# Kernel tuning notes

Measured on AMD Instinct MI355X. Metric: run time of the kernel, lower is better.

The kernel has to match this reference:

```python
import jax, jax.numpy as jnp
import numpy as np

B, LQ, LKV = 4, 512, 8192
Q_DIM, KV_DIM = 1024, 512
QK_CH, V_CH, N_HEADS = 256, 256, 8
EPS = 1e-5


def _layernorm(x, g, b):
    m = jnp.mean(x, axis=-1, keepdims=True)
    v = jnp.mean(jnp.square(x - m), axis=-1, keepdims=True)
    return (x - m) * jax.lax.rsqrt(v + EPS) * g + b


def setup_inputs() -> dict:
    key = jax.random.key(0)
    ks = jax.random.split(key, 8)
    hidden_states = jax.random.normal(ks[0], (B, LQ, Q_DIM), dtype=jnp.float32)
    inputs = jax.random.normal(ks[1], (B, LKV, KV_DIM), dtype=jnp.float32)
    # Linear weights stored as [in, out] for x @ W
    Wq = jax.random.normal(ks[2], (Q_DIM, QK_CH), dtype=jnp.float32) * (1.0 / np.sqrt(Q_DIM))
    Wk = jax.random.normal(ks[3], (KV_DIM, QK_CH), dtype=jnp.float32) * (1.0 / np.sqrt(KV_DIM))
    Wv = jax.random.normal(ks[4], (KV_DIM, V_CH), dtype=jnp.float32) * (1.0 / np.sqrt(KV_DIM))
    bq = jnp.zeros((QK_CH,), jnp.float32)
    bk = jax.random.normal(ks[5], (QK_CH,), dtype=jnp.float32) * 0.02
    bv = jax.random.normal(ks[6], (V_CH,), dtype=jnp.float32) * 0.02
    ln1_g = jnp.ones((Q_DIM,), jnp.float32)
    ln1_b = jnp.zeros((Q_DIM,), jnp.float32)
    ln2_g = jnp.ones((KV_DIM,), jnp.float32)
    ln2_b = jnp.zeros((KV_DIM,), jnp.float32)
    return dict(hidden_states=hidden_states, inputs=inputs,
                ln1_g=ln1_g, ln1_b=ln1_b, ln2_g=ln2_g, ln2_b=ln2_b,
                Wq=Wq, bq=bq, Wk=Wk, bk=bk, Wv=Wv, bv=bv)


def reference(hidden_states, inputs, ln1_g, ln1_b, ln2_g, ln2_b,
              Wq, bq, Wk, bk, Wv, bv):
    H = N_HEADS
    dqk = QK_CH // H
    dv = V_CH // H
    hs = _layernorm(hidden_states, ln1_g, ln1_b)          # [B,LQ,Q_DIM]
    inp = _layernorm(inputs, ln2_g, ln2_b)                # [B,LKV,KV_DIM]
    q = (hs @ Wq + bq).reshape(B, LQ, H, dqk)             # [B,LQ,H,dqk]
    k = (inp @ Wk + bk).reshape(B, LKV, H, dqk)           # [B,LKV,H,dqk]
    v = (inp @ Wv + bv).reshape(B, LKV, H, dv)            # [B,LKV,H,dv]
    scores = jnp.einsum('bqhd,bkhd->bhqk', q, k) / np.sqrt(dqk).astype(np.float32)
    probs = jax.nn.softmax(scores, axis=-1)               # [B,H,LQ,LKV] (materialized, as in torch)
    ctx = jnp.einsum('bhqk,bkhd->bqhd', probs, v)         # [B,LQ,H,dv]
    return ctx.reshape(B, LQ, H * dv)
```

## Files before the change

### kernel.cpp

```cpp
#include <hip/hip_runtime.h>
#include <hip/hip_bf16.h>
#include <math.h>

#define NB    4
#define LQ    512
#define LKV   8192
#define QDIM  1024
#define KVDIM 512
#define NH    8
#define EPS_LN 1e-5f
#define SMAX  12.0f

typedef __attribute__((ext_vector_type(8))) short bf16x8;
typedef __attribute__((ext_vector_type(4))) float f32x4;

static __device__ __forceinline__ ushort f2bf(float x) {
    unsigned int u = __builtin_bit_cast(unsigned int, x);
    u += 0x7FFFu + ((u >> 16) & 1u);
    return (ushort)(u >> 16);
}

#if __has_builtin(__builtin_amdgcn_cvt_pk_bf16_f32)
static __device__ __forceinline__ unsigned int pk_bf16(float a, float b) {
    auto r = __builtin_amdgcn_cvt_pk_bf16_f32(a, b);
    return __builtin_bit_cast(unsigned int, r);
}
#else
static __device__ __forceinline__ unsigned int pk_bf16(float a, float b) {
    return (unsigned int)f2bf(a) | ((unsigned int)f2bf(b) << 16);
}
#endif

#if __has_builtin(__builtin_amdgcn_exp2f)
#define EXP2F(x) __builtin_amdgcn_exp2f(x)
#else
#define EXP2F(x) exp2f(x)
#endif

static __device__ __forceinline__ void interleave_swap(unsigned int &x, unsigned int &y, int lane) {
#if __has_builtin(__builtin_amdgcn_permlane32_swap) && __has_builtin(__builtin_amdgcn_permlane16_swap)
    {
        auto r1 = __builtin_amdgcn_permlane32_swap(x, y, false, false);
        auto r2 = __builtin_amdgcn_permlane16_swap(r1[0], r1[1], false, false);
        x = (unsigned int)r2[0];
        y = (unsigned int)r2[1];
    }
#else
    {
        unsigned int xs = (unsigned int)__shfl_xor((int)x, 32, 64);
        unsigned int ys = (unsigned int)__shfl_xor((int)y, 32, 64);
        unsigned int A2 = (lane & 32) ? ys : x;
        unsigned int C2 = (lane & 32) ? y  : xs;
        unsigned int A2x = (unsigned int)__shfl_xor((int)A2, 16, 64);
        unsigned int C2x = (unsigned int)__shfl_xor((int)C2, 16, 64);
        x = (lane & 16) ? C2x : A2;
        y = (lane & 16) ? C2  : A2x;
    }
#endif
}

static __device__ __forceinline__ void gld_lds16(const ushort* g, ushort* l) {
    __builtin_amdgcn_global_load_lds(
        (const __attribute__((address_space(1))) unsigned int*)g,
        (__attribute__((address_space(3))) unsigned int*)l, 16, 0, 0);
}

template<int K>
static __device__ __forceinline__ void ln_norm_row(
    const float* __restrict__ x, const float* __restrict__ g,
    const float* __restrict__ bta, ushort* __restrict__ y, int row, int lane)
{
    const float* xp = x + (size_t)row * K;
    constexpr int NV = K / 256;
    float4 v[NV];
    float s = 0.f;
#pragma unroll
    for (int i = 0; i < NV; ++i) {
        v[i] = *(const float4*)(xp + lane * 4 + i * 256);
        s += v[i].x + v[i].y + v[i].z + v[i].w;
    }
#pragma unroll
    for (int o = 1; o < 64; o <<= 1) s += __shfl_xor(s, o, 64);
    const float mu = s * (1.0f / K);
    float vs = 0.f;
#pragma unroll
    for (int i = 0; i < NV; ++i) {
        float dx = v[i].x - mu, dy = v[i].y - mu, dz = v[i].z - mu, dw = v[i].w - mu;
        vs += dx * dx + dy * dy + dz * dz + dw * dw;
    }
#pragma unroll
    for (int o = 1; o < 64; o <<= 1) vs += __shfl_xor(vs, o, 64);
    const float rs = rsqrtf(vs * (1.0f / K) + EPS_LN);
#pragma unroll
    for (int i = 0; i < NV; ++i) {
        const float4 gv = *(const float4*)(g   + lane * 4 + i * 256);
        const float4 bv = *(const float4*)(bta + lane * 4 + i * 256);
        uint2 o;
        o.x = pk_bf16((v[i].x - mu) * rs * gv.x + bv.x, (v[i].y - mu) * rs * gv.y + bv.y);
        o.y = pk_bf16((v[i].z - mu) * rs * gv.z + bv.z, (v[i].w - mu) * rs * gv.w + bv.w);
        *(uint2*)(y + (size_t)row * K + lane * 4 + i * 256) = o;
    }
}

static __device__ __forceinline__ void ln_stats_row(
    const float* __restrict__ x, float* __restrict__ mean, float* __restrict__ rstd,
    int row, int lane)
{
    const float* xp = x + (size_t)row * QDIM;
    float4 v[4];
    float s = 0.f;
#pragma unroll
    for (int i = 0; i < 4; ++i) {
        v[i] = *(const float4*)(xp + lane * 4 + i * 256);
        s += v[i].x + v[i].y + v[i].z + v[i].w;
    }
#pragma unroll
    for (int o = 1; o < 64; o <<= 1) s += __shfl_xor(s, o, 64);
    const float mu = s * (1.0f / QDIM);
    float vs = 0.f;
#pragma unroll
    for (int i = 0; i < 4; ++i) {
        float dx = v[i].x - mu, dy = v[i].y - mu, dz = v[i].z - mu, dw = v[i].w - mu;
        vs += dx * dx + dy * dy + dz * dz + dw * dw;
    }
#pragma unroll
    for (int o = 1; o < 64; o <<= 1) vs += __shfl_xor(vs, o, 64);
    if (lane == 0) {
        mean[row] = mu;
        rstd[row] = rsqrtf(vs * (1.0f / QDIM) + EPS_LN);
    }
}

static __device__ __forceinline__ void wt_transpose_body(
    const float* __restrict__ src, ushort* __restrict__ dst, int K,
    int kx, int ny, int t, ushort (*Ts)[72])
{
    const int k0 = kx * 64, n0 = ny * 64;
    const int nl = t & 63;
#pragma unroll
    for (int p = 0; p < 16; ++p) {
        const int kl = p * 4 + (t >> 6);
        Ts[nl][kl] = f2bf(src[(size_t)(k0 + kl) * 256 + n0 + nl]);
    }
    __syncthreads();
    const int ck = (t & 7) * 8;
#pragma unroll
    for (int p = 0; p < 2; ++p) {
        const int rn = p * 32 + (t >> 3);
        *(bf16x8*)(dst + (size_t)(n0 + rn) * K + k0 + ck) = *(const bf16x8*)&Ts[rn][ck];
    }
}

__global__ __launch_bounds__(256) void phaseA_kernel(
    const float* __restrict__ inputs, const float* __restrict__ ln2g,
    const float* __restrict__ ln2b,   ushort* __restrict__ Abf,
    const float* __restrict__ hidden, float* __restrict__ mean_h, float* __restrict__ rstd_h,
    const float* __restrict__ Wq, const float* __restrict__ Wk, const float* __restrict__ Wv,
    ushort* __restrict__ WtQ, ushort* __restrict__ WtKV)
{
    __shared__ ushort Ts[64][72];
    const int bid = blockIdx.x;
    const int t = threadIdx.x;
    const int lane = t & 63;
    if (bid < 8192) {
        ln_norm_row<KVDIM>(inputs, ln2g, ln2b, Abf, bid * 4 + (t >> 6), lane);
    } else if (bid < 8704) {
        ln_stats_row(hidden, mean_h, rstd_h, (bid - 8192) * 4 + (t >> 6), lane);
    } else if (bid < 8768) {
        const int p = bid - 8704;
        wt_transpose_body(Wq, WtQ, QDIM, p & 15, p >> 4, t, Ts);
    } else if (bid < 8800) {
        const int p = bid - 8768;
        wt_transpose_body(Wk, WtKV, KVDIM, p & 7, p >> 3, t, Ts);
    } else {
        const int p = bid - 8800;
        wt_transpose_body(Wv, WtKV + (size_t)256 * KVDIM, KVDIM, p & 7, p >> 3, t, Ts);
    }
}

__global__ __launch_bounds__(256, 3) void phaseB_kernel(
    const ushort* __restrict__ Abf, const ushort* __restrict__ WtKV,
    const float* __restrict__ bk, const float* __restrict__ bv,
    ushort* __restrict__ kb, ushort* __restrict__ vt,
    const float* __restrict__ hidden, const float* __restrict__ mean_h,
    const float* __restrict__ rstd_h,
    const float* __restrict__ ln1g, const float* __restrict__ ln1b,
    const ushort* __restrict__ WtQ, const float* __restrict__ bq,
    ushort* __restrict__ qb, float oscale)
{
    __shared__ __align__(16) ushort SMEM[24576];
    const int bid  = blockIdx.x;
    const int t    = threadIdx.x;
    const int lane = t & 63;
    const int w    = t >> 6;
    const int lq   = lane & 15;
    const int lg   = lane >> 4;
    const int wm   = w >> 1;
    const int wn   = w & 1;

    if (bid < 2048) {
        const int work = ((bid & 7) << 8) | (bid >> 3);
        const int bm = (work >> 2) * 64;
        const int bn = (work & 3) * 128;

        const int srow = t >> 3;
        const int scol = ((t & 7) ^ (srow & 7)) * 8;
        const ushort* gA = Abf  + (size_t)(bm + srow) * KVDIM + scol;
        const ushort* gB = WtKV + (size_t)(bn + srow) * KVDIM + scol;

#define STAGE_KV(buf, k0) do {                                              \
        ushort* a_ = SMEM + (buf) * 4096;                                   \
        ushort* b_ = SMEM + 8192 + (buf) * 8192;                            \
        gld_lds16(gA + (k0),                          a_ + t * 8);          \
        gld_lds16(gA + (size_t)32 * KVDIM + (k0),     a_ + 2048 + t * 8);   \
        gld_lds16(gB + (k0),                          b_ + t * 8);          \
        gld_lds16(gB + (size_t)32 * KVDIM + (k0),     b_ + 2048 + t * 8);   \
        gld_lds16(gB + (size_t)64 * KVDIM + (k0),     b_ + 4096 + t * 8);   \
        gld_lds16(gB + (size_t)96 * KVDIM + (k0),     b_ + 6144 + t * 8);   \
    } while (0)

        f32x4 acc[4][2] = {};
        STAGE_KV(0, 0);
        __syncthreads();
        for (int i = 0; i < 8; ++i) {
            const int cur = i & 1;
            if (i < 7) STAGE_KV(cur ^ 1, (i + 1) * 64);
            const ushort* a_ = SMEM + cur * 4096;
            const ushort* b_ = SMEM + 8192 + cur * 8192;
#pragma unroll
            for (int kh = 0; kh < 2; ++kh) {
                bf16x8 af[4], bf[2];
#pragma unroll
                for (int mt = 0; mt < 4; ++mt) {
                    const int m = mt * 16 + lq;
                    af[mt] = *(const bf16x8*)(a_ + m * 64 + (((lg + 4 * kh) ^ (m & 7)) << 3));
                }
#pragma unroll
                for (int nt = 0; nt < 2; ++nt) {
                    const int n = w * 32 + nt * 16 + lq;
                    bf[nt] = *(const bf16x8*)(b_ + n * 64 + (((lg + 4 * kh) ^ (n & 7)) << 3));
                }
#pragma unroll
                for (int mt = 0; mt < 4; ++mt)
#pragma unroll
                    for (int nt = 0; nt < 2; ++nt)
                        acc[mt][nt] = __builtin_amdgcn_mfma_f32_16x16x32_bf16(af[mt], bf[nt], acc[mt][nt], 0, 0, 0);
            }
            __syncthreads();
        }
#undef STAGE_KV
        const int bidx = bm >> 13;
        const int tokb = bm & 8191;
        const int nc0  = bn + w * 32;

        if (bn < 256) {
            ushort* Cs = SMEM + w * 2560;
#pragma unroll
            for (int nt = 0; nt < 2; ++nt) {
                const int n_l = nt * 16 + lq;
                const float bias = bk[nc0 + n_l];
#pragma unroll
                for (int mt = 0; mt < 4; ++mt)
#pragma unroll
                    for (int r = 0; r < 4; ++r)
                        Cs[(mt * 16 + lg * 4 + r) * 40 + n_l] = f2bf(acc[mt][nt][r] + bias);
            }
            const int r0 = lane >> 2;
            const int ck = (lane & 3) * 8;
            const int h  = nc0 >> 5;
            const size_t obase = (((size_t)(bidx * NH + h) << 13) + tokb) * 32 + ck;
#pragma unroll
            for (int p = 0; p < 4; ++p) {
                const int row = p * 16 + r0;
                *(bf16x8*)(kb + obase + (size_t)row * 32) = *(const bf16x8*)&Cs[row * 40 + ck];
            }
        } else {
            ushort* Cs = SMEM + w * 2560;
#pragma unroll
            for (int nt = 0; nt < 2; ++nt) {
                const int n_l = nt * 16 + lq;
                const float bias = bv[(nc0 - 256) + n_l];
#pragma unroll
                for (int mt = 0; mt < 4; ++mt) {
                    uint2 o;
                    o.x = pk_bf16(acc[mt][nt][0] + bias, acc[mt][nt][1] + bias);
                    o.y = pk_bf16(acc[mt][nt][2] + bias, acc[mt][nt][3] + bias);
                    *(uint2*)&Cs[n_l * 72 + mt * 16 + lg * 4] = o;
                }
            }
            const int r0 = lane >> 3;
            const int cm = (lane & 7) * 8;
            const int nv0 = nc0 - 256;
            const int h  = nv0 >> 5;
            const int tokc = tokb + cm;
#pragma unroll
            for (int p = 0; p < 4; ++p) {
                const int row = p * 8 + r0;
                *(bf16x8*)(vt + ((size_t)(bidx * NH + h) * 32 + row) * LKV + tokc) =
                    *(const bf16x8*)&Cs[row * 72 + cm];
            }
        }
    } else {
        const int p  = bid - 2048;
        const int bm = (p >> 2) * 64;
        const int bn = (p & 3) * 64;
        ushort* As = SMEM;
        ushort* Bs = SMEM + 4096;

        const int srow = t >> 3;
        const int scol = ((t & 7) ^ (srow & 7)) * 8;
        const ushort* gB = WtQ + (size_t)(bn + srow) * QDIM + scol;
        ushort* lB  = Bs + t * 8;
        ushort* lA0 = As + t * 8;
        ushort* lA1 = As + 2048 + t * 8;

        const int r0 = bm + srow;
        const float mu0 = mean_h[r0],      rs0 = rstd_h[r0];
        const float mu1 = mean_h[r0 + 32], rs1 = rstd_h[r0 + 32];
        const float* xA0 = hidden + (size_t)r0 * QDIM + scol;
        const float* xA1 = xA0 + (size_t)32 * QDIM;

        f32x4 acc[2][2] = {};
        for (int k0 = 0; k0 < QDIM; k0 += 64) {
            gld_lds16(gB + k0,                      lB);
            gld_lds16(gB + (size_t)32 * QDIM + k0,  lB + 2048);
            const float4 a0 = *(const float4*)(xA0 + k0);
            const float4 a1 = *(const float4*)(xA0 + k0 + 4);
            const float4 c0 = *(const float4*)(xA1 + k0);
            const float4 c1 = *(const float4*)(xA1 + k0 + 4);
            const float4 g0 = *(const float4*)(ln1g + k0 + scol);
            const float4 g1 = *(const float4*)(ln1g + k0 + scol + 4);
            const float4 d0 = *(const float4*)(ln1b + k0 + scol);
            const float4 d1 = *(const float4*)(ln1b + k0 + scol + 4);
            uint4 w0, w1;
            w0.x = pk_bf16((a0.x - mu0) * rs0 * g0.x + d0.x, (a0.y - mu0) * rs0 * g0.y + d0.y);
            w0.y = pk_bf16((a0.z - mu0) * rs0 * g0.z + d0.z, (a0.w - mu0) * rs0 * g0.w + d0.w);
            w0.z = pk_bf16((a1.x - mu0) * rs0 * g1.x + d1.x, (a1.y - mu0) * rs0 * g1.y + d1.y);
            w0.w = pk_bf16((a1.z - mu0) * rs0 * g1.z + d1.z, (a1.w - mu0) * rs0 * g1.w + d1.w);
            w1.x = pk_bf16((c0.x - mu1) * rs1 * g0.x + d0.x, (c0.y - mu1) * rs1 * g0.y + d0.y);
            w1.y = pk_bf16((c0.z - mu1) * rs1 * g0.z + d0.z, (c0.w - mu1) * rs1 * g0.w + d0.w);
            w1.z = pk_bf16((c1.x - mu1) * rs1 * g1.x + d1.x, (c1.y - mu1) * rs1 * g1.y + d1.y);
            w1.w = pk_bf16((c1.z - mu1) * rs1 * g1.z + d1.z, (c1.w - mu1) * rs1 * g1.w + d1.w);
            *(uint4*)lA0 = w0;
            *(uint4*)lA1 = w1;
            __syncthreads();
#pragma unroll
            for (int kh = 0; kh < 2; ++kh) {
                bf16x8 af[2], bf[2];
#pragma unroll
                for (int mt = 0; mt < 2; ++mt) {
                    const int m = wm * 32 + mt * 16 + lq;
                    af[mt] = *(const bf16x8*)(As + m * 64 + (((lg + 4 * kh) ^ (m & 7)) << 3));
                }
#pragma unroll
                for (int nt = 0; nt < 2; ++nt) {
                    const int n = wn * 32 + nt * 16 + lq;
                    bf[nt] = *(const bf16x8*)(Bs + n * 64 + (((lg + 4 * kh) ^ (n & 7)) << 3));
                }
#pragma unroll
                for (int mt = 0; mt < 2; ++mt)
#pragma unroll
                    for (int nt = 0; nt < 2; ++nt)
                        acc[mt][nt] = __builtin_amdgcn_mfma_f32_16x16x32_bf16(af[mt], bf[nt], acc[mt][nt], 0, 0, 0);
            }
            __syncthreads();
        }

#pragma unroll
        for (int nt = 0; nt < 2; ++nt) {
            const int n = bn + wn * 32 + nt * 16 + lq;
            const int h = n >> 5, d = n & 31;
            const float bias = bq[n];
#pragma unroll
            for (int mt = 0; mt < 2; ++mt) {
                const int m0   = bm + wm * 32 + mt * 16 + lg * 4;
                const int bidx = m0 >> 9;
                const int tok  = m0 & 511;
                const size_t base = (((size_t)(bidx * NH + h) << 9) + tok) * 32 + d;
#pragma unroll
                for (int r = 0; r < 4; ++r)
                    qb[base + (size_t)r * 32] = f2bf((acc[mt][nt][r] + bias) * oscale);
            }
        }
    }
}

#define NQ 8
__global__ __launch_bounds__(256, 2) void attn_mfma_kernel(
    const ushort* __restrict__ Qb,
    const ushort* __restrict__ Kb,
    const ushort* __restrict__ Vt,
    float* __restrict__ Opart,
    float* __restrict__ lpart)
{
    const int bid = blockIdx.x;
    const int xcd = bid & 7;
    const int u   = bid >> 3;
    const int bhw = u >> 4;
    const int r2  = u & 15;
    const int qt  = r2 >> 2;
    const int quarter = r2 & 3;
    const int bh  = (bhw << 3) | xcd;
    const int t = threadIdx.x, w = t >> 6, lane = t & 63;
    const int lq = lane & 15, lg = lane >> 4;

    __shared__ __align__(16) float Ob[2 * 128 * 36];
    __shared__ float lbuf[4][128];

    bf16x8 qfrag[NQ];
    const size_t qbase = ((size_t)bh * LQ + qt * 128) * 32;
#pragma unroll
    for (int n = 0; n < NQ; ++n)
        qfrag[n] = *(const bf16x8*)(Qb + qbase + (size_t)(n * 16 + lq) * 32 + lg * 8);

    const int kv0 = quarter * 2048 + w * 512;
    const ushort* KpA = Kb + ((size_t)bh * LKV + kv0 + lq) * 32 + lg * 8;
    const ushort* VpA = Vt + ((size_t)bh * 32 + lq) * LKV + kv0 + lg * 8;

    f32x4 oacc[2][NQ] = {};
    float l_part[NQ] = {};
    const f32x4 cM = {-SMAX, -SMAX, -SMAX, -SMAX};

    for (int kt = 0; kt < 512; kt += 64) {
        bf16x8 kc[4];
#pragma unroll
        for (int m = 0; m < 4; ++m)
            kc[m] = *(const bf16x8*)(KpA + (size_t)(kt + m * 16) * 32);
        bf16x8 vc[2][2];
#pragma unroll
        for (int dt = 0; dt < 2; ++dt)
#pragma unroll
            for (int z = 0; z < 2; ++z)
                vc[dt][z] = *(const bf16x8*)(VpA + (size_t)(dt * 16) * LKV + kt + z * 32);

#pragma unroll
        for (int z = 0; z < 2; ++z) {
#pragma unroll
            for (int n = 0; n < NQ; ++n) {
                f32x4 s0 = __builtin_amdgcn_mfma_f32_16x16x32_bf16(kc[2 * z],     qfrag[n], cM, 0, 0, 0);
                f32x4 s1 = __builtin_amdgcn_mfma_f32_16x16x32_bf16(kc[2 * z + 1], qfrag[n], cM, 0, 0, 0);
                const float e0 = EXP2F(s0[0]);
                const float e1 = EXP2F(s0[1]);
                const float e2 = EXP2F(s0[2]);
                const float e3 = EXP2F(s0[3]);
                const float f0 = EXP2F(s1[0]);
                const float f1 = EXP2F(s1[1]);
                const float f2 = EXP2F(s1[2]);
                const float f3 = EXP2F(s1[3]);
                l_part[n] += ((e0 + e1) + (e2 + e3)) + ((f0 + f1) + (f2 + f3));
                unsigned int wa = pk_bf16(e0, e1);
                unsigned int wb = pk_bf16(e2, e3);
                unsigned int wc = pk_bf16(f0, f1);
                unsigned int wd = pk_bf16(f2, f3);
                interleave_swap(wa, wc, lane);
                interleave_swap(wb, wd, lane);
                uint4 wv;
                wv.x = wa; wv.y = wb; wv.z = wc; wv.w = wd;
                const bf16x8 pfz = __builtin_bit_cast(bf16x8, wv);
                oacc[0][n] = __builtin_amdgcn_mfma_f32_16x16x32_bf16(vc[0][z], pfz, oacc[0][n], 0, 0, 0);
                oacc[1][n] = __builtin_amdgcn_mfma_f32_16x16x32_bf16(vc[1][z], pfz, oacc[1][n], 0, 0, 0);
            }
        }
    }

#pragma unroll
    for (int n = 0; n < NQ; ++n) {
        l_part[n] += __shfl_xor(l_part[n], 16);
        l_part[n] += __shfl_xor(l_part[n], 32);
    }
    if (lg == 0) {
#pragma unroll
        for (int n = 0; n < NQ; ++n)
            lbuf[w][n * 16 + lq] = l_part[n];
    }
    if (w >= 2) {
#pragma unroll
        for (int n = 0; n < NQ; ++n)
#pragma unroll
            for (int dt = 0; dt < 2; ++dt)
                *(f32x4*)&Ob[((size_t)(w - 2) * 128 + n * 16 + lq) * 36 + dt * 16 + lg * 4] = oacc[dt][n];
    }
    __syncthreads();
    if (w < 2) {
#pragma unroll
        for (int n = 0; n < NQ; ++n)
#pragma unroll
            for (int dt = 0; dt < 2; ++dt) {
                float* p = &Ob[((size_t)w * 128 + n * 16 + lq) * 36 + dt * 16 + lg * 4];
                f32x4 v = *(f32x4*)p;
                v += oacc[dt][n];
                *(f32x4*)p = v;
            }
    }
    __syncthreads();
    {
        const int pidx = (quarter * 32 + bh) * 4 + qt;
        const int q  = t >> 3;
        const int d0 = (t & 7) * 4;
#pragma unroll
        for (int rh = 0; rh < 4; ++rh) {
            const int row = q + rh * 32;
            f32x4 s0 = *(const f32x4*)&Ob[((size_t)row) * 36 + d0];
            f32x4 s1 = *(const f32x4*)&Ob[((size_t)(128 + row)) * 36 + d0];
            s0 += s1;
            *(f32x4*)(Opart + (size_t)pidx * 4096 + row * 32 + d0) = s0;
            if ((t & 7) == 0) {
                float gl = lbuf[0][row] + lbuf[1][row] + lbuf[2][row] + lbuf[3][row];
                lpart[(size_t)pidx * 128 + row] = gl;
            }
        }
    }
}

__global__ __launch_bounds__(256) void attn_combine_kernel(
    const float* __restrict__ Opart, const float* __restrict__ lpart,
    float* __restrict__ Out)
{
    const int cb = blockIdx.x;
    const int bh = cb >> 2, qt = cb & 3;
    const int b = bh >> 3, h = bh & 7;
    const int t = threadIdx.x;
    const int q = t >> 3;
    const int dq = (t & 7) * 4;
#pragma unroll
    for (int rh = 0; rh < 4; ++rh) {
        const int row = q + rh * 32;
        float4 o = {0.f, 0.f, 0.f, 0.f};
        float l = 0.f;
#pragma unroll
        for (int j = 0; j < 4; ++j) {
            const size_t pidx = (size_t)((j * 32 + bh) * 4 + qt);
            const float4 a = *(const float4*)(Opart + pidx * 4096 + row * 32 + dq);
            o.x += a.x; o.y += a.y; o.z += a.z; o.w += a.w;
            l += lpart[pidx * 128 + row];
        }
        const float inv = 1.0f / l;
        o.x *= inv; o.y *= inv; o.z *= inv; o.w *= inv;
        *(float4*)(Out + ((size_t)b * LQ + qt * 128 + row) * 256 + h * 32 + dq) = o;
    }
}

extern "C" void kernel_launch(void* const* d_in, const int* in_sizes, int n_in,
                              void* d_out, int out_size, void* d_ws, size_t ws_size,
                              hipStream_t stream)
{
    const float* hidden = (const float*)d_in[0];
    const float* inputs = (const float*)d_in[1];
    const float* ln1g   = (const float*)d_in[2];
    const float* ln1b   = (const float*)d_in[3];
    const float* ln2g   = (const float*)d_in[4];
    const float* ln2b   = (const float*)d_in[5];
    const float* Wq     = (const float*)d_in[6];
    const float* bq     = (const float*)d_in[7];
    const float* Wk     = (const float*)d_in[8];
    const float* bk     = (const float*)d_in[9];
    const float* Wv     = (const float*)d_in[10];
    const float* bv     = (const float*)d_in[11];
    float* out = (float*)d_out;

    char* wsb = (char*)d_ws;
    ushort* qb     = (ushort*)(wsb);
    ushort* WtKV   = (ushort*)(wsb + (1u << 20));
    ushort* WtQ    = (ushort*)(wsb + (1u << 20) + (512u << 10));
    float*  mean_h = (float*)(wsb + (2u << 20));
    float*  rstd_h = (float*)(wsb + (2u << 20) + 8192);
    ushort* kb     = (ushort*)(wsb + (2u << 20) + 16384);
    ushort* vt     = (ushort*)(wsb + (18u << 20) + 16384);
    ushort* Abf    = (ushort*)(wsb + (34u << 20) + 16384);

    float* Opart = (float*)Abf;
    float* lpart = Opart + (size_t)4 * 32 * 4 * 4096;

    const float oscale = 0.2550540226496112f;

    phaseA_kernel<<<8832, 256, 0, stream>>>(inputs, ln2g, ln2b, Abf,
                                            hidden, mean_h, rstd_h,
                                            Wq, Wk, Wv, WtQ, WtKV);
    phaseB_kernel<<<2176, 256, 0, stream>>>(Abf, WtKV, bk, bv, kb, vt,
                                            hidden, mean_h, rstd_h, ln1g, ln1b,
                                            WtQ, bq, qb, oscale);
    attn_mfma_kernel<<<512, 256, 0, stream>>>(qb, kb, vt, Opart, lpart);
    attn_combine_kernel<<<128, 256, 0, stream>>>(Opart, lpart, out);
}
```

Baseline: 199.2 us.

## Enlarge KV projection tiles to 128x256 with 512-thread blocks

After: 202.9 us. Within noise of the previous version (+1.8%).

```diff
diff --git a/kernel.cpp b/kernel.cpp
--- a/kernel.cpp
+++ b/kernel.cpp
@@ -178,7 +178,7 @@
     }
 }
 
-__global__ __launch_bounds__(256, 3) void phaseB_kernel(
+__global__ __launch_bounds__(512, 2) void phaseB_kernel(
     const ushort* __restrict__ Abf, const ushort* __restrict__ WtKV,
     const float* __restrict__ bk, const float* __restrict__ bv,
     ushort* __restrict__ kb, ushort* __restrict__ vt,
@@ -195,113 +195,111 @@
     const int w    = t >> 6;
     const int lq   = lane & 15;
     const int lg   = lane >> 4;
-    const int wm   = w >> 1;
-    const int wn   = w & 1;
-
-    if (bid < 2048) {
-        const int work = ((bid & 7) << 8) | (bid >> 3);
-        const int bm = (work >> 2) * 64;
-        const int bn = (work & 3) * 128;
-
-        const int srow = t >> 3;
-        const int scol = ((t & 7) ^ (srow & 7)) * 8;
+    const int wm   = w >> 2;
+    const int wn   = w & 3;
+
+    if (bid < 512) {
+        const int work = ((bid & 7) << 6) | (bid >> 3);
+        const int bm = (work >> 1) * 128;
+        const int bn = (work & 1) * 256;
+
+        const int srow = t >> 2;
+        const int scol = ((t & 3) ^ ((t >> 3) & 3)) * 8;
         const ushort* gA = Abf  + (size_t)(bm + srow) * KVDIM + scol;
         const ushort* gB = WtKV + (size_t)(bn + srow) * KVDIM + scol;
 
-#define STAGE_KV(buf, k0) do {                                              \
-        ushort* a_ = SMEM + (buf) * 4096;                                   \
-        ushort* b_ = SMEM + 8192 + (buf) * 8192;                            \
-        gld_lds16(gA + (k0),                          a_ + t * 8);          \
-        gld_lds16(gA + (size_t)32 * KVDIM + (k0),     a_ + 2048 + t * 8);   \
-        gld_lds16(gB + (k0),                          b_ + t * 8);          \
-        gld_lds16(gB + (size_t)32 * KVDIM + (k0),     b_ + 2048 + t * 8);   \
-        gld_lds16(gB + (size_t)64 * KVDIM + (k0),     b_ + 4096 + t * 8);   \
-        gld_lds16(gB + (size_t)96 * KVDIM + (k0),     b_ + 6144 + t * 8);   \
+#define STAGE_KV(buf, k0) do {                                            \
+        ushort* a_ = SMEM + (buf) * 4096;                                 \
+        ushort* b_ = SMEM + 8192 + (buf) * 8192;                          \
+        gld_lds16(gA + (k0),                       a_ + t * 8);           \
+        gld_lds16(gB + (k0),                       b_ + t * 8);           \
+        gld_lds16(gB + (size_t)128 * KVDIM + (k0), b_ + 4096 + t * 8);    \
     } while (0)
 
-        f32x4 acc[4][2] = {};
+        f32x4 acc[4][4] = {};
         STAGE_KV(0, 0);
         __syncthreads();
-        for (int i = 0; i < 8; ++i) {
+        for (int i = 0; i < 16; ++i) {
             const int cur = i & 1;
-            if (i < 7) STAGE_KV(cur ^ 1, (i + 1) * 64);
+            if (i < 15) STAGE_KV(cur ^ 1, (i + 1) * 32);
             const ushort* a_ = SMEM + cur * 4096;
             const ushort* b_ = SMEM + 8192 + cur * 8192;
-#pragma unroll
-            for (int kh = 0; kh < 2; ++kh) {
-                bf16x8 af[4], bf[2];
-#pragma unroll
-                for (int mt = 0; mt < 4; ++mt) {
-                    const int m = mt * 16 + lq;
-                    af[mt] = *(const bf16x8*)(a_ + m * 64 + (((lg + 4 * kh) ^ (m & 7)) << 3));
-                }
-#pragma unroll
-                for (int nt = 0; nt < 2; ++nt) {
-                    const int n = w * 32 + nt * 16 + lq;
-                    bf[nt] = *(const bf16x8*)(b_ + n * 64 + (((lg + 4 * kh) ^ (n & 7)) << 3));
-                }
-#pragma unroll
-                for (int mt = 0; mt < 4; ++mt)
-#pragma unroll
-                    for (int nt = 0; nt < 2; ++nt)
-                        acc[mt][nt] = __builtin_amdgcn_mfma_f32_16x16x32_bf16(af[mt], bf[nt], acc[mt][nt], 0, 0, 0);
-            }
+            bf16x8 af[4], bf[4];
+#pragma unroll
+            for (int mt = 0; mt < 4; ++mt) {
+                const int m = wm * 64 + mt * 16 + lq;
+                af[mt] = *(const bf16x8*)(a_ + m * 32 + ((lg ^ ((m >> 1) & 3)) << 3));
+            }
+#pragma unroll
+            for (int nt = 0; nt < 4; ++nt) {
+                const int n = wn * 64 + nt * 16 + lq;
+                bf[nt] = *(const bf16x8*)(b_ + n * 32 + ((lg ^ ((n >> 1) & 3)) << 3));
+            }
+#pragma unroll
+            for (int mt = 0; mt < 4; ++mt)
+#pragma unroll
+                for (int nt = 0; nt < 4; ++nt)
+                    acc[mt][nt] = __builtin_amdgcn_mfma_f32_16x16x32_bf16(af[mt], bf[nt], acc[mt][nt], 0, 0, 0);
             __syncthreads();
         }
 #undef STAGE_KV
         const int bidx = bm >> 13;
-        const int tokb = bm & 8191;
-        const int nc0  = bn + w * 32;
-
-        if (bn < 256) {
-            ushort* Cs = SMEM + w * 2560;
-#pragma unroll
-            for (int nt = 0; nt < 2; ++nt) {
-                const int n_l = nt * 16 + lq;
-                const float bias = bk[nc0 + n_l];
-#pragma unroll
-                for (int mt = 0; mt < 4; ++mt)
-#pragma unroll
-                    for (int r = 0; r < 4; ++r)
-                        Cs[(mt * 16 + lg * 4 + r) * 40 + n_l] = f2bf(acc[mt][nt][r] + bias);
-            }
-            const int r0 = lane >> 2;
-            const int ck = (lane & 3) * 8;
-            const int h  = nc0 >> 5;
-            const size_t obase = (((size_t)(bidx * NH + h) << 13) + tokb) * 32 + ck;
-#pragma unroll
-            for (int p = 0; p < 4; ++p) {
-                const int row = p * 16 + r0;
-                *(bf16x8*)(kb + obase + (size_t)row * 32) = *(const bf16x8*)&Cs[row * 40 + ck];
+        const int tokb = (bm & 8191) + wm * 64;
+        ushort* Cs = SMEM + w * 2560;
+
+        if (bn == 0) {
+#pragma unroll
+            for (int ch = 0; ch < 2; ++ch) {
+                const int c0 = wn * 64 + ch * 32;
+                const int h  = c0 >> 5;
+#pragma unroll
+                for (int ntr = 0; ntr < 2; ++ntr) {
+                    const int n_l = ntr * 16 + lq;
+                    const float bias = bk[c0 + n_l];
+#pragma unroll
+                    for (int mt = 0; mt < 4; ++mt)
+#pragma unroll
+                        for (int r = 0; r < 4; ++r)
+                            Cs[(mt * 16 + lg * 4 + r) * 40 + n_l] = f2bf(acc[mt][ch * 2 + ntr][r] + bias);
+                }
+                const int r0s = lane >> 2;
+                const int ck  = (lane & 3) * 8;
+                const size_t obase = (((size_t)(bidx * NH + h) << 13) + tokb) * 32 + ck;
+#pragma unroll
+                for (int p = 0; p < 4; ++p) {
+                    const int row = p * 16 + r0s;
+                    *(bf16x8*)(kb + obase + (size_t)row * 32) = *(const bf16x8*)&Cs[row * 40 + ck];
+                }
             }
         } else {
-            ushort* Cs = SMEM + w * 2560;
-#pragma unroll
-            for (int nt = 0; nt < 2; ++nt) {
-                const int n_l = nt * 16 + lq;
-                const float bias = bv[(nc0 - 256) + n_l];
-#pragma unroll
-                for (int mt = 0; mt < 4; ++mt) {
-                    uint2 o;
-                    o.x = pk_bf16(acc[mt][nt][0] + bias, acc[mt][nt][1] + bias);
-                    o.y = pk_bf16(acc[mt][nt][2] + bias, acc[mt][nt][3] + bias);
-                    *(uint2*)&Cs[n_l * 72 + mt * 16 + lg * 4] = o;
+#pragma unroll
+            for (int ch = 0; ch < 2; ++ch) {
+                const int c0 = wn * 64 + ch * 32;
+                const int h  = c0 >> 5;
+#pragma unroll
+                for (int ntr = 0; ntr < 2; ++ntr) {
+                    const int n_l = ntr * 16 + lq;
+                    const float bias = bv[c0 + n_l];
+#pragma unroll
+                    for (int mt = 0; mt < 4; ++mt) {
+                        uint2 o;
+                        o.x = pk_bf16(acc[mt][ch * 2 + ntr][0] + bias, acc[mt][ch * 2 + ntr][1] + bias);
+                        o.y = pk_bf16(acc[mt][ch * 2 + ntr][2] + bias, acc[mt][ch * 2 + ntr][3] + bias);
+                        *(uint2*)&Cs[n_l * 72 + mt * 16 + lg * 4] = o;
+                    }
                 }
-            }
-            const int r0 = lane >> 3;
-            const int cm = (lane & 7) * 8;
-            const int nv0 = nc0 - 256;
-            const int h  = nv0 >> 5;
-            const int tokc = tokb + cm;
-#pragma unroll
-            for (int p = 0; p < 4; ++p) {
-                const int row = p * 8 + r0;
-                *(bf16x8*)(vt + ((size_t)(bidx * NH + h) * 32 + row) * LKV + tokc) =
-                    *(const bf16x8*)&Cs[row * 72 + cm];
+                const int r0s = lane >> 3;
+                const int cm  = (lane & 7) * 8;
+#pragma unroll
+                for (int p = 0; p < 4; ++p) {
+                    const int row = p * 8 + r0s;
+                    *(bf16x8*)(vt + ((size_t)(bidx * NH + h) * 32 + row) * LKV + tokb + cm) =
+                        *(const bf16x8*)&Cs[row * 72 + cm];
+                }
             }
         }
     } else {
-        const int p  = bid - 2048;
+        const int p  = bid - 512;
         const int bm = (p >> 2) * 64;
         const int bn = (p & 3) * 64;
         ushort* As = SMEM;
@@ -310,65 +308,50 @@
         const int srow = t >> 3;
         const int scol = ((t & 7) ^ (srow & 7)) * 8;
         const ushort* gB = WtQ + (size_t)(bn + srow) * QDIM + scol;
-        ushort* lB  = Bs + t * 8;
-        ushort* lA0 = As + t * 8;
-        ushort* lA1 = As + 2048 + t * 8;
+        ushort* lB = Bs + t * 8;
+        ushort* lA = As + t * 8;
 
         const int r0 = bm + srow;
-        const float mu0 = mean_h[r0],      rs0 = rstd_h[r0];
-        const float mu1 = mean_h[r0 + 32], rs1 = rstd_h[r0 + 32];
-        const float* xA0 = hidden + (size_t)r0 * QDIM + scol;
-        const float* xA1 = xA0 + (size_t)32 * QDIM;
-
-        f32x4 acc[2][2] = {};
+        const float mu = mean_h[r0], rs = rstd_h[r0];
+        const float* xA = hidden + (size_t)r0 * QDIM + scol;
+
+        f32x4 acc[2] = {};
         for (int k0 = 0; k0 < QDIM; k0 += 64) {
-            gld_lds16(gB + k0,                      lB);
-            gld_lds16(gB + (size_t)32 * QDIM + k0,  lB + 2048);
-            const float4 a0 = *(const float4*)(xA0 + k0);
-            const float4 a1 = *(const float4*)(xA0 + k0 + 4);
-            const float4 c0 = *(const float4*)(xA1 + k0);
-            const float4 c1 = *(const float4*)(xA1 + k0 + 4);
+            gld_lds16(gB + k0, lB);
+            const float4 a0 = *(const float4*)(xA + k0);
+            const float4 a1 = *(const float4*)(xA + k0 + 4);
             const float4 g0 = *(const float4*)(ln1g + k0 + scol);
             const float4 g1 = *(const float4*)(ln1g + k0 + scol + 4);
             const float4 d0 = *(const float4*)(ln1b + k0 + scol);
             const float4 d1 = *(const float4*)(ln1b + k0 + scol + 4);
-            uint4 w0, w1;
-            w0.x = pk_bf16((a0.x - mu0) * rs0 * g0.x + d0.x, (a0.y - mu0) * rs0 * g0.y + d0.y);
-            w0.y = pk_bf16((a0.z - mu0) * rs0 * g0.z + d0.z, (a0.w - mu0) * rs0 * g0.w + d0.w);
-            w0.z = pk_bf16((a1.x - mu0) * rs0 * g1.x + d1.x, (a1.y - mu0) * rs0 * g1.y + d1.y);
-            w0.w = pk_bf16((a1.z - mu0) * rs0 * g1.z + d1.z, (a1.w - mu0) * rs0 * g1.w + d1.w);
-            w1.x = pk_bf16((c0.x - mu1) * rs1 * g0.x + d0.x, (c0.y - mu1) * rs1 * g0.y + d0.y);
-            w1.y = pk_bf16((c0.z - mu1) * rs1 * g0.z + d0.z, (c0.w - mu1) * rs1 * g0.w + d0.w);
-            w1.z = pk_bf16((c1.x - mu1) * rs1 * g1.x + d1.x, (c1.y - mu1) * rs1 * g1.y + d1.y);
-            w1.w = pk_bf16((c1.z - mu1) * rs1 * g1.z + d1.z, (c1.w - mu1) * rs1 * g1.w + d1.w);
-            *(uint4*)lA0 = w0;
-            *(uint4*)lA1 = w1;
+            uint4 w0;
+            w0.x = pk_bf16((a0.x - mu) * rs * g0.x + d0.x, (a0.y - mu) * rs * g0.y + d0.y);
+            w0.y = pk_bf16((a0.z - mu) * rs * g0.z + d0.z, (a0.w - mu) * rs * g0.w + d0.w);
+            w0.z = pk_bf16((a1.x - mu) * rs * g1.x + d1.x, (a1.y - mu) * rs * g1.y + d1.y);
+            w0.w = pk_bf16((a1.z - mu) * rs * g1.z + d1.z, (a1.w - mu) * rs * g1.w + d1.w);
+            *(uint4*)lA = w0;
             __syncthreads();
 #pragma unroll
             for (int kh = 0; kh < 2; ++kh) {
-                bf16x8 af[2], bf[2];
+                bf16x8 af[2], bfr;
 #pragma unroll
                 for (int mt = 0; mt < 2; ++mt) {
                     const int m = wm * 32 + mt * 16 + lq;
                     af[mt] = *(const bf16x8*)(As + m * 64 + (((lg + 4 * kh) ^ (m & 7)) << 3));
                 }
-#pragma unroll
-                for (int nt = 0; nt < 2; ++nt) {
-                    const int n = wn * 32 + nt * 16 + lq;
-                    bf[nt] = *(const bf16x8*)(Bs + n * 64 + (((lg + 4 * kh) ^ (n & 7)) << 3));
+                {
+                    const int n = wn * 16 + lq;
+                    bfr = *(const bf16x8*)(Bs + n * 64 + (((lg + 4 * kh) ^ (n & 7)) << 3));
                 }
 #pragma unroll
                 for (int mt = 0; mt < 2; ++mt)
-#pragma unroll
-                    for (int nt = 0; nt < 2; ++nt)
-                        acc[mt][nt] = __builtin_amdgcn_mfma_f32_16x16x32_bf16(af[mt], bf[nt], acc[mt][nt], 0, 0, 0);
+                    acc[mt] = __builtin_amdgcn_mfma_f32_16x16x32_bf16(af[mt], bfr, acc[mt], 0, 0, 0);
             }
             __syncthreads();
         }
 
-#pragma unroll
-        for (int nt = 0; nt < 2; ++nt) {
-            const int n = bn + wn * 32 + nt * 16 + lq;
+        {
+            const int n = bn + wn * 16 + lq;
             const int h = n >> 5, d = n & 31;
             const float bias = bq[n];
 #pragma unroll
@@ -379,7 +362,7 @@
                 const size_t base = (((size_t)(bidx * NH + h) << 9) + tok) * 32 + d;
 #pragma unroll
                 for (int r = 0; r < 4; ++r)
-                    qb[base + (size_t)r * 32] = f2bf((acc[mt][nt][r] + bias) * oscale);
+                    qb[base + (size_t)r * 32] = f2bf((acc[mt][r] + bias) * oscale);
             }
         }
     }
@@ -576,9 +559,9 @@
     phaseA_kernel<<<8832, 256, 0, stream>>>(inputs, ln2g, ln2b, Abf,
                                             hidden, mean_h, rstd_h,
                                             Wq, Wk, Wv, WtQ, WtKV);
-    phaseB_kernel<<<2176, 256, 0, stream>>>(Abf, WtKV, bk, bv, kb, vt,
-                                            hidden, mean_h, rstd_h, ln1g, ln1b,
-                                            WtQ, bq, qb, oscale);
+    phaseB_kernel<<<640, 512, 0, stream>>>(Abf, WtKV, bk, bv, kb, vt,
+                                           hidden, mean_h, rstd_h, ln1g, ln1b,
+                                           WtQ, bq, qb, oscale);
     attn_mfma_kernel<<<512, 256, 0, stream>>>(qb, kb, vt, Opart, lpart);
     attn_combine_kernel<<<128, 256, 0, stream>>>(Opart, lpart, out);
 }
```
